# Kernel tuning notes

Measured on AMD Instinct MI355X. Metric: run time of the kernel, lower is better.

The kernel has to match this reference:

```python
import jax, jax.numpy as jnp
import numpy as np

HEAD_DIM = 128
NUM_BUCKETS = 32
MAX_DISTANCE = 128


def _rel_pos_bucket(seq_len):
    # T5 causal relative-position bucketing (lucidrains flash-pytorch version)
    pos = jnp.arange(seq_len)
    rel = pos[None, :] - pos[:, None]          # k_pos - q_pos
    n = jnp.maximum(-rel, 0)                   # causal: only past distances
    max_exact = NUM_BUCKETS // 2
    is_small = n < max_exact
    n_safe = jnp.maximum(n, 1).astype(jnp.float32)
    val_large = max_exact + (
        jnp.log(n_safe / max_exact) / np.log(MAX_DISTANCE / max_exact)
        * (NUM_BUCKETS - max_exact)
    ).astype(jnp.int32)
    val_large = jnp.minimum(val_large, NUM_BUCKETS - 1)
    return jnp.where(is_small, n, val_large)   # (S, S) int32


def setup_inputs() -> dict:
    key = jax.random.key(0)
    ks = jax.random.split(key, 10)
    B, S, D, I = 4, 2048, 768, 1536
    s = 0.02
    return {
        "x": jax.random.normal(ks[0], (B, S, D), jnp.float32),
        "v_W": jax.random.normal(ks[1], (D, I), jnp.float32) * s,
        "v_b": jnp.zeros((I,), jnp.float32),
        "g_W": jax.random.normal(ks[2], (D, I), jnp.float32) * s,
        "g_b": jnp.zeros((I,), jnp.float32),
        "in_W": jax.random.normal(ks[3], (D, HEAD_DIM), jnp.float32) * s,
        "in_b": jnp.zeros((HEAD_DIM,), jnp.float32),
        "q_gamma": jax.random.normal(ks[4], (HEAD_DIM,), jnp.float32) * s,
        "q_beta": jnp.zeros((HEAD_DIM,), jnp.float32),
        "k_gamma": jax.random.normal(ks[5], (HEAD_DIM,), jnp.float32) * s,
        "k_beta": jnp.zeros((HEAD_DIM,), jnp.float32),
        "out_W": jax.random.normal(ks[6], (I, D), jnp.float32) * s,
        "out_b": jnp.zeros((D,), jnp.float32),
        "rel_emb": jax.random.normal(ks[7], (NUM_BUCKETS, 1), jnp.float32) * s,
    }


def reference(x, v_W, v_b, g_W, g_b, in_W, in_b,
              q_gamma, q_beta, k_gamma, k_beta, out_W, out_b, rel_emb):
    silu = jax.nn.silu
    S = x.shape[1]
    v = silu(x @ v_W + v_b)                    # (B, S, I)
    gate = silu(x @ g_W + g_b)                 # (B, S, I)
    base = silu(x @ in_W + in_b)               # (B, S, 128)
    q = base * q_gamma + q_beta
    k = base * k_gamma + k_beta
    # scores scaled by sqrt(v dim) per torch code (v.size(-1) = inner_dim)
    attn = jnp.einsum('bns,bms->bnm', q, k) / jnp.sqrt(jnp.float32(v.shape[-1]))
    bias = rel_emb[_rel_pos_bucket(S), 0] * np.sqrt(HEAD_DIM)  # (S, S)
    attn = attn + bias
    causal = jnp.triu(jnp.ones((S, S), bool), 1)
    attn = jnp.where(causal, 0.0, attn)        # masked_fill to 0 before relu^2
    attn = jnp.square(jax.nn.relu(attn))       # ReLU^2 attention (no softmax)
    o = jnp.einsum('bnm,bme->bne', attn, v) * gate
    return o @ out_W + out_b                   # (B, S, D)
```

## Files before the change

### kernel.cpp

```cpp
#include <hip/hip_runtime.h>


typedef short short8 __attribute__((ext_vector_type(8)));
typedef float f32x4 __attribute__((ext_vector_type(4)));
typedef unsigned short us4 __attribute__((ext_vector_type(4)));
typedef float fl4 __attribute__((ext_vector_type(4)));

__device__ __forceinline__ unsigned short f2bf(float f) {
  unsigned u = __builtin_bit_cast(unsigned, f);
  u += 0x7FFFu + ((u >> 16) & 1u);
  return (unsigned short)(u >> 16);
}
__device__ __forceinline__ float bf2f(unsigned short b) {
  return __builtin_bit_cast(float, ((unsigned)b) << 16);
}
__device__ __forceinline__ float silu_f(float x) { return x / (1.0f + __expf(-x)); }

__device__ __forceinline__ void gl_lds(const unsigned short* gp, unsigned short* lp) {
  __builtin_amdgcn_global_load_lds((const __attribute__((address_space(1))) void*)gp,
                                   (__attribute__((address_space(3))) void*)lp, 16, 0, 0);
}

__device__ __forceinline__ void stage_tile(const unsigned short* __restrict__ g,
                                           int row_stride, int r0, int ko,
                                           unsigned short* lds, int w, int l) {
#pragma unroll
  for (int c = 0; c < 4; ++c) {
    int e = ((w * 4 + c) << 9) + l * 8;
    gl_lds(g + (size_t)(r0 + (e >> 6)) * row_stride + (ko + (e & 63)), lds + e);
  }
}

__device__ __forceinline__ void mfma_step(const unsigned short* As, const unsigned short* Bs,
                                          f32x4 acc[4][4], int wm, int wn, int quad, int lc) {
#pragma unroll
  for (int kk = 0; kk < 2; ++kk) {
    short8 af[4], bfr[4];
#pragma unroll
    for (int i = 0; i < 4; ++i)
      af[i] = *(const short8*)&As[(wm + i * 16 + lc) * 64 + kk * 32 + quad * 8];
#pragma unroll
    for (int j = 0; j < 4; ++j)
      bfr[j] = *(const short8*)&Bs[(wn + j * 16 + lc) * 64 + kk * 32 + quad * 8];
#pragma unroll
    for (int i = 0; i < 4; ++i)
#pragma unroll
      for (int j = 0; j < 4; ++j)
        acc[i][j] = __builtin_amdgcn_mfma_f32_16x16x32_bf16(af[i], bfr[j], acc[i][j], 0, 0, 0);
  }
}

__global__ __launch_bounds__(256) void g123_k(
    const unsigned short* __restrict__ X,
    const unsigned short* __restrict__ Wst,
    unsigned short* __restrict__ vt,
    unsigned short* __restrict__ gateT,
    unsigned short* __restrict__ wq,
    unsigned short* __restrict__ wk,
    const float* __restrict__ v_b, const float* __restrict__ g_b,
    const float* __restrict__ in_b, const float* __restrict__ q_g,
    const float* __restrict__ q_be, const float* __restrict__ k_g,
    const float* __restrict__ k_be) {
  __shared__ unsigned short As[128 * 64];
  __shared__ unsigned short Bs[128 * 64];
  const int t = threadIdx.x, l = t & 63, w = t >> 6;
  const int id = blockIdx.x;
  const int xcd = id & 7, rest = id >> 3;
  const int n = rest % 25, m = (rest / 25) * 8 + xcd;
  const int m0 = m * 128, n0 = n * 128;
  const int wm = (w >> 1) * 64, wn = (w & 1) * 64;
  const int quad = l >> 4, lr = quad * 4, lc = l & 15;

  f32x4 acc[4][4] = {};
  for (int ko = 0; ko < 768; ko += 64) {
    stage_tile(X, 768, m0, ko, As, w, l);
    stage_tile(Wst, 768, n0, ko, Bs, w, l);
    __syncthreads();
    mfma_step(As, Bs, acc, wm, wn, quad, lc);
    __syncthreads();
  }

#pragma unroll
  for (int i = 0; i < 4; ++i) {
    const int gm = m0 + wm + i * 16 + lr;
#pragma unroll
    for (int j = 0; j < 4; ++j) {
      const int gn = n0 + wn + j * 16 + lc;
      f32x4 a = acc[i][j];
      if (n0 < 1536) {
        float bv = v_b[gn];
        us4 pk;
#pragma unroll
        for (int r = 0; r < 4; ++r) pk[r] = f2bf(silu_f(a[r] + bv));
        size_t off = (size_t)(gm >> 11) * (1536 * 2048) + (size_t)gn * 2048 + (gm & 2047);
        *(us4*)&vt[off] = pk;
      } else if (n0 < 3072) {
        float bv = g_b[gn - 1536];
        us4 pk;
#pragma unroll
        for (int r = 0; r < 4; ++r) pk[r] = f2bf(silu_f(a[r] + bv));
        *(us4*)&gateT[(size_t)(gn - 1536) * 8192 + gm] = pk;
      } else {
        int h = gn - 3072;
        float bb = in_b[h], qg = q_g[h], qb = q_be[h], kg = k_g[h], kb = k_be[h];
#pragma unroll
        for (int r = 0; r < 4; ++r) {
          float s = silu_f(a[r] + bb);
          wq[(size_t)(gm + r) * 128 + h] = f2bf(s * qg + qb);
          wk[(size_t)(gm + r) * 128 + h] = f2bf(s * kg + kb);
        }
      }
    }
  }
}

__global__ __launch_bounds__(256) void scores_k(
    const unsigned short* __restrict__ wk, const unsigned short* __restrict__ wq,
    unsigned short* __restrict__ P, const float* __restrict__ btab) {
  __shared__ unsigned short As[128 * 64];
  __shared__ unsigned short Bs[128 * 64];
  const int t = threadIdx.x, l = t & 63, w = t >> 6;
  const int z = blockIdx.z;
  int ti = blockIdx.x;
  int r = (int)((sqrtf((float)(8 * ti + 1)) - 1.0f) * 0.5f);
  if ((r + 1) * (r + 2) / 2 <= ti) ++r;
  int c = ti - r * (r + 1) / 2;
  const int m0 = c * 128, n0 = r * 128;
  const unsigned short* A = wk + (size_t)z * 2048 * 128;
  const unsigned short* Bt = wq + (size_t)z * 2048 * 128;
  unsigned short* Pz = P + (size_t)z * 2048 * 2048;
  const int wm = (w >> 1) * 64, wn = (w & 1) * 64;
  const int quad = l >> 4, lr = quad * 4, lc = l & 15;

  f32x4 acc[4][4] = {};
  for (int ko = 0; ko < 128; ko += 64) {
    stage_tile(A, 128, m0, ko, As, w, l);
    stage_tile(Bt, 128, n0, ko, Bs, w, l);
    __syncthreads();
    mfma_step(As, Bs, acc, wm, wn, quad, lc);
    __syncthreads();
  }
  const float SCALE = 0.025515518153991442f;
#pragma unroll
  for (int i = 0; i < 4; ++i) {
    const int gm = m0 + wm + i * 16 + lr;
#pragma unroll
    for (int j = 0; j < 4; ++j) {
      const int gn = n0 + wn + j * 16 + lc;
      us4 pk;
#pragma unroll
      for (int r2 = 0; r2 < 4; ++r2) {
        int mm = gm + r2;
        float v = 0.0f;
        if (mm <= gn) {
          float tt = fmaf(acc[i][j][r2], SCALE, btab[gn - mm]);
          tt = fmaxf(tt, 0.0f);
          v = tt * tt;
        }
        pk[r2] = f2bf(v);
      }
      *(us4*)&Pz[(size_t)gn * 2048 + gm] = pk;
    }
  }
}

__global__ __launch_bounds__(256) void og_k(
    const unsigned short* __restrict__ Vt,
    const unsigned short* __restrict__ P,
    const unsigned short* __restrict__ gateT,
    unsigned short* __restrict__ og) {
  __shared__ unsigned short As[128 * 64];
  __shared__ unsigned short Bs[128 * 64];
  const int t = threadIdx.x, l = t & 63, w = t >> 6;
  const int id = blockIdx.x;
  const int bblk = id / 96, rr = id % 96;
  const int xcd = rr & 7, mi = rr >> 3;
  const int half = xcd >> 2, z = xcd & 3;
  const int nt = 15 - 2 * bblk - (half ^ (bblk & 1));
  const int m0 = mi * 128;
  const int n0 = nt * 128;
  const int kend = n0 + 128;
  const unsigned short* A = Vt + (size_t)z * 1536 * 2048;
  const unsigned short* B = P + (size_t)z * 2048 * 2048;
  const int wm = (w >> 1) * 64, wn = (w & 1) * 64;
  const int quad = l >> 4, lr = quad * 4, lc = l & 15;

  f32x4 acc[4][4] = {};
  for (int ko = 0; ko < kend; ko += 64) {
    stage_tile(A, 2048, m0, ko, As, w, l);
    stage_tile(B, 2048, n0, ko, Bs, w, l);
    __syncthreads();
    mfma_step(As, Bs, acc, wm, wn, quad, lc);
    __syncthreads();
  }
#pragma unroll
  for (int i = 0; i < 4; ++i) {
    const int gm = m0 + wm + i * 16 + lr;
#pragma unroll
    for (int j = 0; j < 4; ++j) {
      const int gn = n0 + wn + j * 16 + lc;
      us4 pk;
#pragma unroll
      for (int r2 = 0; r2 < 4; ++r2) {
        float g = bf2f(gateT[(size_t)(gm + r2) * 8192 + z * 2048 + gn]);
        pk[r2] = f2bf(acc[i][j][r2] * g);
      }
      *(us4*)&og[((size_t)z * 2048 + gn) * 1536 + gm] = pk;
    }
  }
}

__global__ __launch_bounds__(256) void gout_k(
    const unsigned short* __restrict__ A,
    const unsigned short* __restrict__ Bt,
    float* __restrict__ out, const float* __restrict__ o_b) {
  __shared__ unsigned short As[128 * 64];
  __shared__ unsigned short Bs[128 * 64];
  const int t = threadIdx.x, l = t & 63, w = t >> 6;
  const int id = blockIdx.x;
  const int xcd = id & 7, rest = id >> 3;
  const int m = rest % 6, n = (rest / 6) * 8 + xcd;
  const int m0 = m * 128, n0 = n * 128;
  const int wm = (w >> 1) * 64, wn = (w & 1) * 64;
  const int quad = l >> 4, lr = quad * 4, lc = l & 15;

  f32x4 acc[4][4] = {};
  for (int ko = 0; ko < 1536; ko += 64) {
    stage_tile(A, 1536, m0, ko, As, w, l);
    stage_tile(Bt, 1536, n0, ko, Bs, w, l);
    __syncthreads();
    mfma_step(As, Bs, acc, wm, wn, quad, lc);
    __syncthreads();
  }
#pragma unroll
  for (int i = 0; i < 4; ++i) {
    const int gm = m0 + wm + i * 16 + lr;
#pragma unroll
    for (int j = 0; j < 4; ++j) {
      const int gn = n0 + wn + j * 16 + lc;
      fl4 ob = *(const fl4*)&o_b[gm];
      fl4 res;
#pragma unroll
      for (int r2 = 0; r2 < 4; ++r2) res[r2] = acc[i][j][r2] + ob[r2];
      *(fl4*)&out[(size_t)gn * 768 + gm] = res;
    }
  }
}

__global__ void cvt_bf16(const float* __restrict__ in, unsigned short* __restrict__ out, int n) {
  int i = (blockIdx.x * blockDim.x + threadIdx.x) * 4;
  if (i < n) {
    fl4 v = *(const fl4*)&in[i];
    us4 o;
#pragma unroll
    for (int r = 0; r < 4; ++r) o[r] = f2bf(v[r]);
    *(us4*)&out[i] = o;
  }
}

__global__ void transpose_cvt4(const float* __restrict__ s0, unsigned short* __restrict__ d0,
                               const float* __restrict__ s1, unsigned short* __restrict__ d1,
                               const float* __restrict__ s2, unsigned short* __restrict__ d2,
                               const float* __restrict__ s3, unsigned short* __restrict__ d3) {
  __shared__ float tile[32][33];
  const float* in;
  unsigned short* out;
  int K_, N_, bxm, bym;
  switch (blockIdx.z) {
    case 0: in = s0; out = d0; K_ = 768; N_ = 1536; bxm = 48; bym = 24; break;
    case 1: in = s1; out = d1; K_ = 768; N_ = 1536; bxm = 48; bym = 24; break;
    case 2: in = s2; out = d2; K_ = 768; N_ = 128;  bxm = 4;  bym = 24; break;
    default: in = s3; out = d3; K_ = 1536; N_ = 768; bxm = 24; bym = 48; break;
  }
  if ((int)blockIdx.x >= bxm || (int)blockIdx.y >= bym) return;
  int bn = blockIdx.x * 32, bk = blockIdx.y * 32;
  int tx = threadIdx.x, ty = threadIdx.y;
#pragma unroll
  for (int i2 = 0; i2 < 32; i2 += 8)
    tile[ty + i2][tx] = in[(size_t)(bk + ty + i2) * N_ + (bn + tx)];
  __syncthreads();
#pragma unroll
  for (int i2 = 0; i2 < 32; i2 += 8)
    out[(size_t)(bn + ty + i2) * K_ + (bk + tx)] = f2bf(tile[tx][ty + i2]);
}

__global__ void build_bias(const float* __restrict__ rel_emb, float* __restrict__ tab) {
  int d = blockIdx.x * blockDim.x + threadIdx.x;
  if (d < 2048) {
    int bucket;
    if (d < 16) {
      bucket = d;
    } else {
      float n = (float)d;
      int vl = 16 + (int)((logf(n * 0.0625f) / logf(8.0f)) * 16.0f);
      bucket = vl < 31 ? vl : 31;
    }
    tab[d] = rel_emb[bucket] * 11.3137085f;
  }
}

extern "C" void kernel_launch(void* const* d_in, const int* in_sizes, int n_in,
                              void* d_out, int out_size, void* d_ws, size_t ws_size,
                              hipStream_t stream) {
  const float* x    = (const float*)d_in[0];
  const float* vW   = (const float*)d_in[1];
  const float* v_b  = (const float*)d_in[2];
  const float* gW   = (const float*)d_in[3];
  const float* g_b  = (const float*)d_in[4];
  const float* inW  = (const float*)d_in[5];
  const float* in_b = (const float*)d_in[6];
  const float* q_g  = (const float*)d_in[7];
  const float* q_be = (const float*)d_in[8];
  const float* k_g  = (const float*)d_in[9];
  const float* k_be = (const float*)d_in[10];
  const float* oW   = (const float*)d_in[11];
  const float* o_b  = (const float*)d_in[12];
  const float* rel  = (const float*)d_in[13];

  char* p = (char*)d_ws;
  auto alloc = [&](size_t bytes) -> char* {
    char* r = p;
    p += (bytes + 255) & ~(size_t)255;
    return r;
  };
  unsigned short* x_bf   = (unsigned short*)alloc(8192ull * 768 * 2);
  unsigned short* wstack = (unsigned short*)alloc(3200ull * 768 * 2);
  unsigned short* vWt  = wstack;
  unsigned short* gWt  = wstack + 1536ull * 768;
  unsigned short* inWt = wstack + 3072ull * 768;
  unsigned short* oWt  = (unsigned short*)alloc(768ull * 1536 * 2);
  unsigned short* wq   = (unsigned short*)alloc(8192ull * 128 * 2);
  unsigned short* wk   = (unsigned short*)alloc(8192ull * 128 * 2);
  unsigned short* vt   = (unsigned short*)alloc(4ull * 1536 * 2048 * 2);
  unsigned short* gateT= (unsigned short*)alloc(1536ull * 8192 * 2);
  unsigned short* P    = (unsigned short*)alloc(4ull * 2048 * 2048 * 2);
  unsigned short* og   = (unsigned short*)alloc(8192ull * 1536 * 2);
  float* btab          = (float*)alloc(2048 * 4);

  cvt_bf16<<<dim3(6144), dim3(256), 0, stream>>>(x, x_bf, 8192 * 768);
  transpose_cvt4<<<dim3(48, 48, 4), dim3(32, 8), 0, stream>>>(vW, vWt, gW, gWt, inW, inWt, oW, oWt);
  build_bias<<<dim3(8), dim3(256), 0, stream>>>(rel, btab);

  g123_k<<<dim3(1600), 256, 0, stream>>>(x_bf, wstack, vt, gateT, wq, wk,
                                         v_b, g_b, in_b, q_g, q_be, k_g, k_be);
  scores_k<<<dim3(136, 1, 4), 256, 0, stream>>>(wk, wq, P, btab);
  og_k<<<dim3(768), 256, 0, stream>>>(vt, P, gateT, og);
  gout_k<<<dim3(384), 256, 0, stream>>>(oWt, og, (float*)d_out, o_b);
}
```

Measured before the change: 319.6 us.

## Double-buffer LDS staging in GEMMs, single-shot scores load, halve gout tile

Adds double-buffered LDS tiles to the projection, attention-value and output GEMMs. The next K-slice is issued with async global-to-LDS loads while MFMAs run on the current one, which removes one barrier per iteration and overlaps memory with compute. The scores kernel now loads the full 128-wide K in one go with a single barrier. The output GEMM uses 64-row M tiles and twice the blocks to improve occupancy and load balance. LDS use per block doubles, which may lower occupancy.

After: 336.8 us. 1.05x slower.

```diff
diff --git a/kernel.cpp b/kernel.cpp
--- a/kernel.cpp
+++ b/kernel.cpp
@@ -16,23 +16,32 @@
 }
 __device__ __forceinline__ float silu_f(float x) { return x / (1.0f + __expf(-x)); }
 
-__device__ __forceinline__ void gl_lds(const unsigned short* gp, unsigned short* lp) {
+__device__ __forceinline__ void gl_lds16(const void* gp, void* lp) {
   __builtin_amdgcn_global_load_lds((const __attribute__((address_space(1))) void*)gp,
                                    (__attribute__((address_space(3))) void*)lp, 16, 0, 0);
 }
 
-__device__ __forceinline__ void stage_tile(const unsigned short* __restrict__ g,
+__device__ __forceinline__ void stage_bf(const unsigned short* __restrict__ g,
+                                         int row_stride, int r0, int ko,
+                                         unsigned short* lds, int w, int l) {
+#pragma unroll
+  for (int c = 0; c < 4; ++c) {
+    int e = ((w * 4 + c) << 9) + l * 8;
+    gl_lds16(g + (size_t)(r0 + (e >> 6)) * row_stride + (ko + (e & 63)), lds + e);
+  }
+}
+__device__ __forceinline__ void stage_bf64(const unsigned short* __restrict__ g,
                                            int row_stride, int r0, int ko,
                                            unsigned short* lds, int w, int l) {
 #pragma unroll
-  for (int c = 0; c < 4; ++c) {
-    int e = ((w * 4 + c) << 9) + l * 8;
-    gl_lds(g + (size_t)(r0 + (e >> 6)) * row_stride + (ko + (e & 63)), lds + e);
-  }
-}
-
-__device__ __forceinline__ void mfma_step(const unsigned short* As, const unsigned short* Bs,
-                                          f32x4 acc[4][4], int wm, int wn, int quad, int lc) {
+  for (int c = 0; c < 2; ++c) {
+    int e = ((w * 2 + c) << 9) + l * 8;
+    gl_lds16(g + (size_t)(r0 + (e >> 6)) * row_stride + (ko + (e & 63)), lds + e);
+  }
+}
+
+__device__ __forceinline__ void mfma_bf(const unsigned short* As, const unsigned short* Bs,
+                                        f32x4 acc[4][4], int wm, int wn, int quad, int lc) {
 #pragma unroll
   for (int kk = 0; kk < 2; ++kk) {
     short8 af[4], bfr[4];
@@ -61,8 +70,8 @@
     const float* __restrict__ in_b, const float* __restrict__ q_g,
     const float* __restrict__ q_be, const float* __restrict__ k_g,
     const float* __restrict__ k_be) {
-  __shared__ unsigned short As[128 * 64];
-  __shared__ unsigned short Bs[128 * 64];
+  __shared__ unsigned short As[2][128 * 64];
+  __shared__ unsigned short Bs[2][128 * 64];
   const int t = threadIdx.x, l = t & 63, w = t >> 6;
   const int id = blockIdx.x;
   const int xcd = id & 7, rest = id >> 3;
@@ -72,13 +81,18 @@
   const int quad = l >> 4, lr = quad * 4, lc = l & 15;
 
   f32x4 acc[4][4] = {};
-  for (int ko = 0; ko < 768; ko += 64) {
-    stage_tile(X, 768, m0, ko, As, w, l);
-    stage_tile(Wst, 768, n0, ko, Bs, w, l);
+  stage_bf(X, 768, m0, 0, As[0], w, l);
+  stage_bf(Wst, 768, n0, 0, Bs[0], w, l);
+  __syncthreads();
+  int cur = 0;
+  for (int tt = 1; tt < 12; ++tt) {
+    stage_bf(X, 768, m0, tt * 64, As[cur ^ 1], w, l);
+    stage_bf(Wst, 768, n0, tt * 64, Bs[cur ^ 1], w, l);
+    mfma_bf(As[cur], Bs[cur], acc, wm, wn, quad, lc);
     __syncthreads();
-    mfma_step(As, Bs, acc, wm, wn, quad, lc);
-    __syncthreads();
-  }
+    cur ^= 1;
+  }
+  mfma_bf(As[cur], Bs[cur], acc, wm, wn, quad, lc);
 
 #pragma unroll
   for (int i = 0; i < 4; ++i) {
@@ -117,8 +131,8 @@
 __global__ __launch_bounds__(256) void scores_k(
     const unsigned short* __restrict__ wk, const unsigned short* __restrict__ wq,
     unsigned short* __restrict__ P, const float* __restrict__ btab) {
-  __shared__ unsigned short As[128 * 64];
-  __shared__ unsigned short Bs[128 * 64];
+  __shared__ unsigned short As[128 * 128];
+  __shared__ unsigned short Bs[128 * 128];
   const int t = threadIdx.x, l = t & 63, w = t >> 6;
   const int z = blockIdx.z;
   int ti = blockIdx.x;
@@ -132,14 +146,35 @@
   const int wm = (w >> 1) * 64, wn = (w & 1) * 64;
   const int quad = l >> 4, lr = quad * 4, lc = l & 15;
 
+#pragma unroll
+  for (int cc = 0; cc < 8; ++cc) {
+    int e = ((w * 8 + cc) << 9) + l * 8;
+    gl_lds16(A + (size_t)(m0 + (e >> 7)) * 128 + (e & 127), As + e);
+  }
+#pragma unroll
+  for (int cc = 0; cc < 8; ++cc) {
+    int e = ((w * 8 + cc) << 9) + l * 8;
+    gl_lds16(Bt + (size_t)(n0 + (e >> 7)) * 128 + (e & 127), Bs + e);
+  }
+  __syncthreads();
+
   f32x4 acc[4][4] = {};
-  for (int ko = 0; ko < 128; ko += 64) {
-    stage_tile(A, 128, m0, ko, As, w, l);
-    stage_tile(Bt, 128, n0, ko, Bs, w, l);
-    __syncthreads();
-    mfma_step(As, Bs, acc, wm, wn, quad, lc);
-    __syncthreads();
-  }
+#pragma unroll
+  for (int kk = 0; kk < 4; ++kk) {
+    short8 af[4], bfr[4];
+#pragma unroll
+    for (int i = 0; i < 4; ++i)
+      af[i] = *(const short8*)&As[(wm + i * 16 + lc) * 128 + kk * 32 + quad * 8];
+#pragma unroll
+    for (int j = 0; j < 4; ++j)
+      bfr[j] = *(const short8*)&Bs[(wn + j * 16 + lc) * 128 + kk * 32 + quad * 8];
+#pragma unroll
+    for (int i = 0; i < 4; ++i)
+#pragma unroll
+      for (int j = 0; j < 4; ++j)
+        acc[i][j] = __builtin_amdgcn_mfma_f32_16x16x32_bf16(af[i], bfr[j], acc[i][j], 0, 0, 0);
+  }
+
   const float SCALE = 0.025515518153991442f;
 #pragma unroll
   for (int i = 0; i < 4; ++i) {
@@ -169,8 +204,8 @@
     const unsigned short* __restrict__ P,
     const unsigned short* __restrict__ gateT,
     unsigned short* __restrict__ og) {
-  __shared__ unsigned short As[128 * 64];
-  __shared__ unsigned short Bs[128 * 64];
+  __shared__ unsigned short As[2][128 * 64];
+  __shared__ unsigned short Bs[2][128 * 64];
   const int t = threadIdx.x, l = t & 63, w = t >> 6;
   const int id = blockIdx.x;
   const int bblk = id / 96, rr = id % 96;
@@ -179,20 +214,26 @@
   const int nt = 15 - 2 * bblk - (half ^ (bblk & 1));
   const int m0 = mi * 128;
   const int n0 = nt * 128;
-  const int kend = n0 + 128;
+  const int T = (n0 + 128) >> 6;
   const unsigned short* A = Vt + (size_t)z * 1536 * 2048;
   const unsigned short* B = P + (size_t)z * 2048 * 2048;
   const int wm = (w >> 1) * 64, wn = (w & 1) * 64;
   const int quad = l >> 4, lr = quad * 4, lc = l & 15;
 
   f32x4 acc[4][4] = {};
-  for (int ko = 0; ko < kend; ko += 64) {
-    stage_tile(A, 2048, m0, ko, As, w, l);
-    stage_tile(B, 2048, n0, ko, Bs, w, l);
+  stage_bf(A, 2048, m0, 0, As[0], w, l);
+  stage_bf(B, 2048, n0, 0, Bs[0], w, l);
+  __syncthreads();
+  int cur = 0;
+  for (int tt = 1; tt < T; ++tt) {
+    stage_bf(A, 2048, m0, tt * 64, As[cur ^ 1], w, l);
+    stage_bf(B, 2048, n0, tt * 64, Bs[cur ^ 1], w, l);
+    mfma_bf(As[cur], Bs[cur], acc, wm, wn, quad, lc);
     __syncthreads();
-    mfma_step(As, Bs, acc, wm, wn, quad, lc);
-    __syncthreads();
-  }
+    cur ^= 1;
+  }
+  mfma_bf(As[cur], Bs[cur], acc, wm, wn, quad, lc);
+
 #pragma unroll
   for (int i = 0; i < 4; ++i) {
     const int gm = m0 + wm + i * 16 + lr;
@@ -214,26 +255,60 @@
     const unsigned short* __restrict__ A,
     const unsigned short* __restrict__ Bt,
     float* __restrict__ out, const float* __restrict__ o_b) {
-  __shared__ unsigned short As[128 * 64];
-  __shared__ unsigned short Bs[128 * 64];
+  __shared__ unsigned short As[2][64 * 64];
+  __shared__ unsigned short Bs[2][128 * 64];
   const int t = threadIdx.x, l = t & 63, w = t >> 6;
   const int id = blockIdx.x;
   const int xcd = id & 7, rest = id >> 3;
-  const int m = rest % 6, n = (rest / 6) * 8 + xcd;
-  const int m0 = m * 128, n0 = n * 128;
-  const int wm = (w >> 1) * 64, wn = (w & 1) * 64;
+  const int m = rest % 12, ng = rest / 12;
+  const int m0 = m * 64, n0 = (ng * 8 + xcd) * 128;
+  const int wm = (w >> 1) * 32, wn = (w & 1) * 64;
   const int quad = l >> 4, lr = quad * 4, lc = l & 15;
 
-  f32x4 acc[4][4] = {};
-  for (int ko = 0; ko < 1536; ko += 64) {
-    stage_tile(A, 1536, m0, ko, As, w, l);
-    stage_tile(Bt, 1536, n0, ko, Bs, w, l);
+  f32x4 acc[2][4] = {};
+  stage_bf64(A, 1536, m0, 0, As[0], w, l);
+  stage_bf(Bt, 1536, n0, 0, Bs[0], w, l);
+  __syncthreads();
+  int cur = 0;
+  for (int tt = 1; tt < 24; ++tt) {
+    stage_bf64(A, 1536, m0, tt * 64, As[cur ^ 1], w, l);
+    stage_bf(Bt, 1536, n0, tt * 64, Bs[cur ^ 1], w, l);
+#pragma unroll
+    for (int kk = 0; kk < 2; ++kk) {
+      short8 af[2], bfr[4];
+#pragma unroll
+      for (int i = 0; i < 2; ++i)
+        af[i] = *(const short8*)&As[cur][(wm + i * 16 + lc) * 64 + kk * 32 + quad * 8];
+#pragma unroll
+      for (int j = 0; j < 4; ++j)
+        bfr[j] = *(const short8*)&Bs[cur][(wn + j * 16 + lc) * 64 + kk * 32 + quad * 8];
+#pragma unroll
+      for (int i = 0; i < 2; ++i)
+#pragma unroll
+        for (int j = 0; j < 4; ++j)
+          acc[i][j] = __builtin_amdgcn_mfma_f32_16x16x32_bf16(af[i], bfr[j], acc[i][j], 0, 0, 0);
+    }
     __syncthreads();
-    mfma_step(As, Bs, acc, wm, wn, quad, lc);
-    __syncthreads();
-  }
-#pragma unroll
-  for (int i = 0; i < 4; ++i) {
+    cur ^= 1;
+  }
+#pragma unroll
+  for (int kk = 0; kk < 2; ++kk) {
+    short8 af[2], bfr[4];
+#pragma unroll
+    for (int i = 0; i < 2; ++i)
+      af[i] = *(const short8*)&As[cur][(wm + i * 16 + lc) * 64 + kk * 32 + quad * 8];
+#pragma unroll
+    for (int j = 0; j < 4; ++j)
+      bfr[j] = *(const short8*)&Bs[cur][(wn + j * 16 + lc) * 64 + kk * 32 + quad * 8];
+#pragma unroll
+    for (int i = 0; i < 2; ++i)
+#pragma unroll
+      for (int j = 0; j < 4; ++j)
+        acc[i][j] = __builtin_amdgcn_mfma_f32_16x16x32_bf16(af[i], bfr[j], acc[i][j], 0, 0, 0);
+  }
+
+#pragma unroll
+  for (int i = 0; i < 2; ++i) {
     const int gm = m0 + wm + i * 16 + lr;
 #pragma unroll
     for (int j = 0; j < 4; ++j) {
@@ -345,5 +420,5 @@
                                          v_b, g_b, in_b, q_g, q_be, k_g, k_be);
   scores_k<<<dim3(136, 1, 4), 256, 0, stream>>>(wk, wq, P, btab);
   og_k<<<dim3(768), 256, 0, stream>>>(vt, P, gateT, og);
-  gout_k<<<dim3(384), 256, 0, stream>>>(oWt, og, (float*)d_out, o_b);
-}
+  gout_k<<<dim3(768), 256, 0, stream>>>(oWt, og, (float*)d_out, o_b);
+}
```
